# Kernel tuning notes

Hardware: AMD Instinct MI355X
Metric: run time of the kernel (lower is better)

Reference implementation:

```python
import math
import jax, jax.numpy as jnp
import numpy as np

B, N, D, H = 4, 2048, 512, 8
HD = D // H


def setup_inputs() -> dict:
    key = jax.random.key(0)
    ks = jax.random.split(key, 7)
    w_scale = 1.0 / math.sqrt(D)  # keep logits in a sane range (like default init)
    return {
        "q": jax.random.normal(ks[0], (B, N, D), dtype=jnp.float32),
        "mask": jax.random.randint(ks[1], (B, N), 0, 2) == 1,  # True = masked key
        "attn_bias": jax.random.normal(ks[2], (B, N, N), dtype=jnp.float32),
        "Wq": jax.random.normal(ks[3], (D, D), dtype=jnp.float32) * w_scale,
        "Wk": jax.random.normal(ks[4], (D, D), dtype=jnp.float32) * w_scale,
        "Wv": jax.random.normal(ks[5], (D, D), dtype=jnp.float32) * w_scale,
        "Wo": jax.random.normal(ks[6], (D, D), dtype=jnp.float32) * w_scale,
    }


def _heads(v):
    # [B, N, D] -> [H, B, N, HD]  (mirrors reshape + movedim(-2, 0))
    b, n, d = v.shape
    return v.reshape(b, n, H, HD).transpose(2, 0, 1, 3)


def reference(q, mask, attn_bias, Wq, Wk, Wv, Wo):
    # Linear projections (torch Linear: x @ W.T)
    qh = _heads(q @ Wq.T)
    kh = _heads(q @ Wk.T)   # self-attention: h defaults to q
    vh = _heads(q @ Wv.T)
    # scores: [H, B, Nq, Nk]
    scores = jnp.einsum("hbqd,hbkd->hbqk", qh, kh) / math.sqrt(HD)
    scores = scores + attn_bias[None]                     # broadcast over heads
    scores = jnp.where(mask[None, :, None, :], -jnp.inf, scores)
    attn = jax.nn.softmax(scores, axis=-1)
    out = jnp.einsum("hbqk,hbkd->hbqd", attn, vh)         # [H, B, Nq, HD]
    out = out.transpose(1, 2, 0, 3).reshape(q.shape[0], q.shape[1], D)
    return out @ Wo.T
```

## Files before the change

kernel.cpp:

```cpp
#include <hip/hip_runtime.h>
#include <stdint.h>


typedef __attribute__((ext_vector_type(8))) short short8;
typedef __attribute__((ext_vector_type(4))) short short4v;
typedef __attribute__((ext_vector_type(4))) float f32x4;

#define DEV static __device__ __forceinline__

constexpr int Bc = 4, Nc = 2048, Dc = 512, Hc = 8, HDc = 64;
constexpr int Mc = Bc * Nc;
constexpr int QKVNc = 3 * Dc;
constexpr float L2E = 1.44269504f;

DEV short bf16cast(float f) {
  return (short)__builtin_bit_cast(unsigned short, (__bf16)f);
}
DEV unsigned cvt_pk_bf16(float a, float b) {
  unsigned short lb = __builtin_bit_cast(unsigned short, (__bf16)a);
  unsigned short hb = __builtin_bit_cast(unsigned short, (__bf16)b);
  return (unsigned)lb | ((unsigned)hb << 16);
}
DEV unsigned pack_shorts(short a, short b) {
  return (unsigned)(unsigned short)a | ((unsigned)(unsigned short)b << 16);
}
DEV short8 cvt8(float4 a, float4 b) {
  union { short8 s; uint4 u; } r;
  r.u.x = cvt_pk_bf16(a.x, a.y); r.u.y = cvt_pk_bf16(a.z, a.w);
  r.u.z = cvt_pk_bf16(b.x, b.y); r.u.w = cvt_pk_bf16(b.z, b.w);
  return r.s;
}
DEV float fast_exp2(float x) {
#if __has_builtin(__builtin_amdgcn_exp2f)
  return __builtin_amdgcn_exp2f(x);
#else
  return exp2f(x);
#endif
}
DEV void permswap32(unsigned& a, unsigned& b) {
  asm volatile("v_permlane32_swap_b32 %0, %1" : "+v"(a), "+v"(b));
}

__global__ void cvtw_kernel(const float* __restrict__ Wq, const float* __restrict__ Wk,
                            const float* __restrict__ Wv, const float* __restrict__ Wo,
                            short* __restrict__ Wqkv, short* __restrict__ Wob,
                            const void* __restrict__ mask, float* __restrict__ mf) {
  if (blockIdx.x == 1024) {
    __shared__ int flag;
    if (threadIdx.x == 0) flag = 0;
    __syncthreads();
    const uchar4* m4 = (const uchar4*)mask;
    int acc = 0;
    for (int i = threadIdx.x; i < 2048; i += 256) {
      uchar4 v = m4[i];
      acc |= (int)v.y | (int)v.z | (int)v.w;
    }
    if (acc) atomicOr(&flag, 1);
    __syncthreads();
    int isbyte = flag;
    for (int i = threadIdx.x; i < Bc * Nc; i += 256) {
      int v = isbyte ? (int)((const unsigned char*)mask)[i] : ((const int*)mask)[i];
      mf[i] = v ? -1e30f : 0.0f;
    }
    return;
  }
  int which = blockIdx.x >> 8;
  int j = (blockIdx.x & 255) * 256 + threadIdx.x;
  const float* src = which == 0 ? Wq : which == 1 ? Wk : which == 2 ? Wv : Wo;
  short* dst = (which == 3) ? Wob : Wqkv + which * (Dc * Dc);
  float4 v = ((const float4*)src)[j];
  short4v o = { bf16cast(v.x), bf16cast(v.y), bf16cast(v.z), bf16cast(v.w) };
  ((short4v*)dst)[j] = o;
}

template<bool A_F32, bool OUT_F32>
__global__ __launch_bounds__(256, 2) void gemm_bt(const void* __restrict__ Av,
                                                  const short* __restrict__ Bm,
                                                  void* __restrict__ Cv,
                                                  int M, int N, int K,
                                                  int qcols, float cscale) {
  __shared__ __align__(16) short At[128 * 72];
  __shared__ __align__(16) short Bt[128 * 72];
  const int tid = threadIdx.x, lane = tid & 63, wv = tid >> 6;
  const int quad = lane >> 4, l16 = lane & 15;
  const int mbase = blockIdx.y * 128, nbase = blockIdx.x * 128;
  const int wr = (wv >> 1) * 64, wc = (wv & 1) * 64;
  const float scale = (nbase < qcols) ? cscale : 1.0f;
  f32x4 acc[4][4] = {};
  float4 apf[4][2]; short8 aph[4], bpre[4];
#pragma unroll
  for (int i = 0; i < 4; i++) {
    int flat = i * 256 + tid, row = flat >> 3, ch8 = (flat & 7) * 8;
    if (A_F32) {
      const float* Af = (const float*)Av;
      apf[i][0] = *(const float4*)&Af[(size_t)(mbase + row) * K + ch8];
      apf[i][1] = *(const float4*)&Af[(size_t)(mbase + row) * K + ch8 + 4];
    } else {
      aph[i] = *(const short8*)&((const short*)Av)[(size_t)(mbase + row) * K + ch8];
    }
    bpre[i] = *(const short8*)&Bm[(size_t)(nbase + row) * K + ch8];
  }
  for (int k0 = 0; k0 < K; k0 += 64) {
    __syncthreads();
#pragma unroll
    for (int i = 0; i < 4; i++) {
      int flat = i * 256 + tid, row = flat >> 3, ch8 = (flat & 7) * 8;
      *(short8*)&At[row * 72 + ch8] = A_F32 ? cvt8(apf[i][0], apf[i][1]) : aph[i];
      *(short8*)&Bt[row * 72 + ch8] = bpre[i];
    }
    if (k0 + 64 < K) {
#pragma unroll
      for (int i = 0; i < 4; i++) {
        int flat = i * 256 + tid, row = flat >> 3, ch8 = (flat & 7) * 8;
        if (A_F32) {
          const float* Af = (const float*)Av;
          apf[i][0] = *(const float4*)&Af[(size_t)(mbase + row) * K + k0 + 64 + ch8];
          apf[i][1] = *(const float4*)&Af[(size_t)(mbase + row) * K + k0 + 64 + ch8 + 4];
        } else {
          aph[i] = *(const short8*)&((const short*)Av)[(size_t)(mbase + row) * K + k0 + 64 + ch8];
        }
        bpre[i] = *(const short8*)&Bm[(size_t)(nbase + row) * K + k0 + 64 + ch8];
      }
    }
    __syncthreads();
#pragma unroll
    for (int s = 0; s < 2; s++) {
      short8 af[4], bf[4];
#pragma unroll
      for (int t = 0; t < 4; t++) {
        af[t] = *(short8*)&At[(wr + t * 16 + l16) * 72 + quad * 8 + s * 32];
        bf[t] = *(short8*)&Bt[(wc + t * 16 + l16) * 72 + quad * 8 + s * 32];
      }
#pragma unroll
      for (int mt = 0; mt < 4; mt++)
#pragma unroll
        for (int nt = 0; nt < 4; nt++)
          acc[mt][nt] = __builtin_amdgcn_mfma_f32_16x16x32_bf16(af[mt], bf[nt], acc[mt][nt], 0, 0, 0);
    }
  }
#pragma unroll
  for (int mt = 0; mt < 4; mt++)
#pragma unroll
    for (int nt = 0; nt < 4; nt++)
#pragma unroll
      for (int r = 0; r < 4; r++) {
        int row = mbase + wr + mt * 16 + quad * 4 + r;
        int col = nbase + wc + nt * 16 + l16;
        float v = acc[mt][nt][r] * scale;
        if (OUT_F32) ((float*)Cv)[(size_t)row * N + col] = v;
        else         ((short*)Cv)[(size_t)row * N + col] = bf16cast(v);
      }
}

__global__ __launch_bounds__(512, 2) void attn_kernel(const short* __restrict__ QKV,
                                                      const float* __restrict__ bias,
                                                      const float* __restrict__ maskf,
                                                      short* __restrict__ Aout) {
  __shared__ __align__(16) short Kt[2][64 * 64];
  __shared__ __align__(16) short Vt[2][64 * 64];
  __shared__ __align__(16) float mlds[Nc];
  const int tid = threadIdx.x, lane = tid & 63, wv = tid >> 6;
  const int quad = lane >> 4, l16 = lane & 15;
  const int qt = blockIdx.x & 15, h = (blockIdx.x >> 4) & 7, b = (int)(blockIdx.x >> 7);
  const int qrow0 = qt * 128;
  const int qglob = qrow0 + wv * 16 + l16;
  const float* biasrow = bias + ((size_t)b * Nc + qglob) * Nc;

  ((float4*)mlds)[tid] = ((const float4*)(maskf + b * Nc))[tid];

  short8 qf[2];
  {
    const short* qp = QKV + (size_t)(b * Nc + qglob) * QKVNc + h * HDc + quad * 8;
    qf[0] = *(const short8*)qp;
    qf[1] = *(const short8*)(qp + 32);
  }

  const int vp = tid & 31, vq = tid >> 5;
  const int vperm = (vp & 25) | ((vp & 4) >> 1) | ((vp & 2) << 1);
  const int krow = tid >> 3, kchunk = tid & 7;
  const int kwofs = krow * 64 + ((kchunk ^ (krow & 7)) << 3);
  const short* Kbase = QKV + Dc + h * HDc;
  const short* Vbase = QKV + 2 * Dc + h * HDc;

  short8 kpre; short4v v0pre, v1pre; float4 bpre[4];
  kpre  = *(const short8*)&Kbase[(size_t)(b * Nc + krow) * QKVNc + kchunk * 8];
  v0pre = *(const short4v*)&Vbase[(size_t)(b * Nc + 2 * vp) * QKVNc + 4 * vq];
  v1pre = *(const short4v*)&Vbase[(size_t)(b * Nc + 2 * vp + 1) * QKVNc + 4 * vq];
#pragma unroll
  for (int t = 0; t < 4; t++) bpre[t] = *(const float4*)&biasrow[t * 16 + quad * 4];

  const short ONEB = (short)0x3F80;
  const short8 ones = { ONEB, ONEB, ONEB, ONEB, ONEB, ONEB, ONEB, ONEB };

  f32x4 oacc[4] = {};
  f32x4 sumacc = {};

  for (int kt = 0; kt < 32; kt++) {
    const int cur = kt & 1;
    const int kb = kt * 64;
    const int kbn = ((kt + 1) & 31) * 64;

    *(short8*)&Kt[cur][kwofs] = kpre;
#pragma unroll
    for (int j = 0; j < 4; j++) {
      int hd = 4 * vq + j;
      *(unsigned*)&Vt[cur][hd * 64 + (((vperm >> 2) ^ (hd & 7)) << 3) + 2 * (vperm & 3)] =
          pack_shorts(v0pre[j], v1pre[j]);
    }
    __syncthreads();

    f32x4 sacc[4];
#pragma unroll
    for (int t = 0; t < 4; t++) {
      float4 mv = *(const float4*)&mlds[kb + t * 16 + quad * 4];
      sacc[t][0] = __builtin_fmaf(bpre[t].x, L2E, mv.x);
      sacc[t][1] = __builtin_fmaf(bpre[t].y, L2E, mv.y);
      sacc[t][2] = __builtin_fmaf(bpre[t].z, L2E, mv.z);
      sacc[t][3] = __builtin_fmaf(bpre[t].w, L2E, mv.w);
    }

    kpre  = *(const short8*)&Kbase[(size_t)(b * Nc + kbn + krow) * QKVNc + kchunk * 8];
    v0pre = *(const short4v*)&Vbase[(size_t)(b * Nc + kbn + 2 * vp) * QKVNc + 4 * vq];
    v1pre = *(const short4v*)&Vbase[(size_t)(b * Nc + kbn + 2 * vp + 1) * QKVNc + 4 * vq];
#pragma unroll
    for (int t = 0; t < 4; t++) bpre[t] = *(const float4*)&biasrow[kbn + t * 16 + quad * 4];

#pragma unroll
    for (int s = 0; s < 2; s++)
#pragma unroll
      for (int t = 0; t < 4; t++) {
        short8 kf = *(short8*)&Kt[cur][(t * 16 + l16) * 64 + (((quad + 4 * s) ^ (l16 & 7)) << 3)];
        sacc[t] = __builtin_amdgcn_mfma_f32_16x16x32_bf16(kf, qf[s], sacc[t], 0, 0, 0);
      }

    unsigned pw[4][2];
#pragma unroll
    for (int t = 0; t < 4; t++) {
      float p0 = fast_exp2(sacc[t][0]);
      float p1 = fast_exp2(sacc[t][1]);
      float p2 = fast_exp2(sacc[t][2]);
      float p3 = fast_exp2(sacc[t][3]);
      pw[t][0] = cvt_pk_bf16(p0, p1);
      pw[t][1] = cvt_pk_bf16(p2, p3);
    }
    permswap32(pw[0][0], pw[1][0]); permswap32(pw[0][1], pw[1][1]);
    permswap32(pw[2][0], pw[3][0]); permswap32(pw[2][1], pw[3][1]);
    union { unsigned u[4]; short8 s; }
        pf0{{pw[0][0], pw[0][1], pw[1][0], pw[1][1]}},
        pf1{{pw[2][0], pw[2][1], pw[3][0], pw[3][1]}};

#pragma unroll
    for (int s = 0; s < 2; s++) {
      short8 pf = s ? pf1.s : pf0.s;
      sumacc = __builtin_amdgcn_mfma_f32_16x16x32_bf16(pf, ones, sumacc, 0, 0, 0);
#pragma unroll
      for (int t = 0; t < 4; t++) {
        short8 vf = *(short8*)&Vt[cur][(t * 16 + l16) * 64 + (((quad + 4 * s) ^ (l16 & 7)) << 3)];
        oacc[t] = __builtin_amdgcn_mfma_f32_16x16x32_bf16(pf, vf, oacc[t], 0, 0, 0);
      }
    }
  }

#pragma unroll
  for (int r = 0; r < 4; r++) {
    float inv = 1.0f / sumacc[r];
    int row = b * Nc + qrow0 + wv * 16 + quad * 4 + r;
#pragma unroll
    for (int t = 0; t < 4; t++)
      Aout[(size_t)row * Dc + h * HDc + t * 16 + l16] = bf16cast(oacc[t][r] * inv);
  }
}

extern "C" void kernel_launch(void* const* d_in, const int* in_sizes, int n_in,
                              void* d_out, int out_size, void* d_ws, size_t ws_size,
                              hipStream_t stream) {
  const float* q    = (const float*)d_in[0];
  const void*  mask = d_in[1];
  const float* bias = (const float*)d_in[2];
  const float* Wq   = (const float*)d_in[3];
  const float* Wk   = (const float*)d_in[4];
  const float* Wv   = (const float*)d_in[5];
  const float* Wo   = (const float*)d_in[6];
  float* out = (float*)d_out;

  char* ws = (char*)d_ws;
  short* Wqkv = (short*)ws;  ws += (size_t)QKVNc * Dc * 2;
  short* Wob  = (short*)ws;  ws += (size_t)Dc * Dc * 2;
  float* mf   = (float*)ws;  ws += (size_t)Bc * Nc * 4;
  short* QKV  = (short*)ws;  ws += (size_t)Mc * QKVNc * 2;
  short* aout = (short*)ws;  ws += (size_t)Mc * Dc * 2;

  cvtw_kernel<<<dim3(1025), dim3(256), 0, stream>>>(Wq, Wk, Wv, Wo, Wqkv, Wob, mask, mf);

  gemm_bt<true, false><<<dim3(QKVNc / 128, Mc / 128), dim3(256), 0, stream>>>(
      (const void*)q, Wqkv, (void*)QKV, Mc, QKVNc, Dc, Dc, 0.125f * L2E);
  attn_kernel<<<dim3(Bc * Hc * 16), dim3(512), 0, stream>>>(QKV, bias, mf, aout);
  gemm_bt<false, true><<<dim3(Dc / 128, Mc / 128), dim3(256), 0, stream>>>(
      (const void*)aout, Wob, (void*)out, Mc, Dc, Dc, 0, 1.0f);
}
```

Baseline: 276.9 us.

## Process two query sub-tiles per wave in attention, halving block threads

The attention kernel now runs 4 waves of 256 threads, each handling 32 query rows as two 16-row MFMA sub-tiles, so each K/V fragment read from LDS feeds two MFMAs. K/V staging loads are widened to 16-byte vectors per thread. Bias loads are no longer prefetched one iteration ahead but issued inside the loop after the barrier, and the bias add moves after the QK MFMA. Mask preparation is split into its own single-block kernel. This raises register pressure and drops bias prefetch latency hiding, which can reduce occupancy or stall on the bias stream.

```diff
diff --git a/kernel.cpp b/kernel.cpp
--- a/kernel.cpp
+++ b/kernel.cpp
@@ -43,27 +43,7 @@
 
 __global__ void cvtw_kernel(const float* __restrict__ Wq, const float* __restrict__ Wk,
                             const float* __restrict__ Wv, const float* __restrict__ Wo,
-                            short* __restrict__ Wqkv, short* __restrict__ Wob,
-                            const void* __restrict__ mask, float* __restrict__ mf) {
-  if (blockIdx.x == 1024) {
-    __shared__ int flag;
-    if (threadIdx.x == 0) flag = 0;
-    __syncthreads();
-    const uchar4* m4 = (const uchar4*)mask;
-    int acc = 0;
-    for (int i = threadIdx.x; i < 2048; i += 256) {
-      uchar4 v = m4[i];
-      acc |= (int)v.y | (int)v.z | (int)v.w;
-    }
-    if (acc) atomicOr(&flag, 1);
-    __syncthreads();
-    int isbyte = flag;
-    for (int i = threadIdx.x; i < Bc * Nc; i += 256) {
-      int v = isbyte ? (int)((const unsigned char*)mask)[i] : ((const int*)mask)[i];
-      mf[i] = v ? -1e30f : 0.0f;
-    }
-    return;
-  }
+                            short* __restrict__ Wqkv, short* __restrict__ Wob) {
   int which = blockIdx.x >> 8;
   int j = (blockIdx.x & 255) * 256 + threadIdx.x;
   const float* src = which == 0 ? Wq : which == 1 ? Wk : which == 2 ? Wv : Wo;
@@ -71,6 +51,25 @@
   float4 v = ((const float4*)src)[j];
   short4v o = { bf16cast(v.x), bf16cast(v.y), bf16cast(v.z), bf16cast(v.w) };
   ((short4v*)dst)[j] = o;
+}
+
+__global__ void maskprep_kernel(const void* __restrict__ mask, float* __restrict__ mf) {
+  __shared__ int flag;
+  if (threadIdx.x == 0) flag = 0;
+  __syncthreads();
+  const uchar4* m4 = (const uchar4*)mask;
+  int acc = 0;
+  for (int i = threadIdx.x; i < 2048; i += 1024) {
+    uchar4 v = m4[i];
+    acc |= (int)v.y | (int)v.z | (int)v.w;
+  }
+  if (acc) atomicOr(&flag, 1);
+  __syncthreads();
+  int isbyte = flag;
+  for (int i = threadIdx.x; i < Bc * Nc; i += 1024) {
+    int v = isbyte ? (int)((const unsigned char*)mask)[i] : ((const int*)mask)[i];
+    mf[i] = v ? -1e30f : 0.0f;
+  }
 }
 
 template<bool A_F32, bool OUT_F32>
@@ -152,7 +151,7 @@
       }
 }
 
-__global__ __launch_bounds__(512, 2) void attn_kernel(const short* __restrict__ QKV,
+__global__ __launch_bounds__(256, 2) void attn_kernel(const short* __restrict__ QKV,
                                                       const float* __restrict__ bias,
                                                       const float* __restrict__ maskf,
                                                       short* __restrict__ Aout) {
@@ -163,112 +162,137 @@
   const int quad = lane >> 4, l16 = lane & 15;
   const int qt = blockIdx.x & 15, h = (blockIdx.x >> 4) & 7, b = (int)(blockIdx.x >> 7);
   const int qrow0 = qt * 128;
-  const int qglob = qrow0 + wv * 16 + l16;
-  const float* biasrow = bias + ((size_t)b * Nc + qglob) * Nc;
-
-  ((float4*)mlds)[tid] = ((const float4*)(maskf + b * Nc))[tid];
-
-  short8 qf[2];
+  const int q0 = qrow0 + wv * 32 + l16;
+  const float* biasq0 = bias + ((size_t)b * Nc + q0) * Nc;
+  const float* biasq1 = biasq0 + (size_t)16 * Nc;
+
+  ((float4*)mlds)[tid]       = ((const float4*)(maskf + b * Nc))[tid];
+  ((float4*)mlds)[tid + 256] = ((const float4*)(maskf + b * Nc))[tid + 256];
+
+  short8 qf[2][2];
   {
-    const short* qp = QKV + (size_t)(b * Nc + qglob) * QKVNc + h * HDc + quad * 8;
-    qf[0] = *(const short8*)qp;
-    qf[1] = *(const short8*)(qp + 32);
-  }
-
+    const short* qp0 = QKV + (size_t)(b * Nc + q0) * QKVNc + h * HDc + quad * 8;
+    qf[0][0] = *(const short8*)qp0;
+    qf[0][1] = *(const short8*)(qp0 + 32);
+    const short* qp1 = qp0 + (size_t)16 * QKVNc;
+    qf[1][0] = *(const short8*)qp1;
+    qf[1][1] = *(const short8*)(qp1 + 32);
+  }
+
+  const int krow = tid >> 2, kch0 = (tid & 3) * 2;
+  const int kw0 = krow * 64 + ((kch0 ^ (krow & 7)) << 3);
+  const int kw1 = krow * 64 + (((kch0 + 1) ^ (krow & 7)) << 3);
   const int vp = tid & 31, vq = tid >> 5;
   const int vperm = (vp & 25) | ((vp & 4) >> 1) | ((vp & 2) << 1);
-  const int krow = tid >> 3, kchunk = tid & 7;
-  const int kwofs = krow * 64 + ((kchunk ^ (krow & 7)) << 3);
+  const int vwbase = (((vperm >> 2)) << 3) + 2 * (vperm & 3);
   const short* Kbase = QKV + Dc + h * HDc;
   const short* Vbase = QKV + 2 * Dc + h * HDc;
 
-  short8 kpre; short4v v0pre, v1pre; float4 bpre[4];
-  kpre  = *(const short8*)&Kbase[(size_t)(b * Nc + krow) * QKVNc + kchunk * 8];
-  v0pre = *(const short4v*)&Vbase[(size_t)(b * Nc + 2 * vp) * QKVNc + 4 * vq];
-  v1pre = *(const short4v*)&Vbase[(size_t)(b * Nc + 2 * vp + 1) * QKVNc + 4 * vq];
-#pragma unroll
-  for (int t = 0; t < 4; t++) bpre[t] = *(const float4*)&biasrow[t * 16 + quad * 4];
+  short8 kpre0, kpre1, v0pre, v1pre;
+  {
+    const short* kp = &Kbase[(size_t)(b * Nc + krow) * QKVNc + kch0 * 8];
+    kpre0 = *(const short8*)kp;
+    kpre1 = *(const short8*)(kp + 8);
+    v0pre = *(const short8*)&Vbase[(size_t)(b * Nc + 2 * vp) * QKVNc + vq * 8];
+    v1pre = *(const short8*)&Vbase[(size_t)(b * Nc + 2 * vp + 1) * QKVNc + vq * 8];
+  }
 
   const short ONEB = (short)0x3F80;
   const short8 ones = { ONEB, ONEB, ONEB, ONEB, ONEB, ONEB, ONEB, ONEB };
 
-  f32x4 oacc[4] = {};
-  f32x4 sumacc = {};
+  f32x4 oacc[2][4] = {};
+  f32x4 sumacc[2] = {};
 
   for (int kt = 0; kt < 32; kt++) {
     const int cur = kt & 1;
     const int kb = kt * 64;
     const int kbn = ((kt + 1) & 31) * 64;
 
-    *(short8*)&Kt[cur][kwofs] = kpre;
-#pragma unroll
-    for (int j = 0; j < 4; j++) {
-      int hd = 4 * vq + j;
-      *(unsigned*)&Vt[cur][hd * 64 + (((vperm >> 2) ^ (hd & 7)) << 3) + 2 * (vperm & 3)] =
+    *(short8*)&Kt[cur][kw0] = kpre0;
+    *(short8*)&Kt[cur][kw1] = kpre1;
+#pragma unroll
+    for (int j = 0; j < 8; j++) {
+      int hd = vq * 8 + j;
+      *(unsigned*)&Vt[cur][hd * 64 + (vwbase ^ ((hd & 7) << 3))] =
           pack_shorts(v0pre[j], v1pre[j]);
     }
     __syncthreads();
 
-    f32x4 sacc[4];
+    {
+      const short* kp = &Kbase[(size_t)(b * Nc + kbn + krow) * QKVNc + kch0 * 8];
+      kpre0 = *(const short8*)kp;
+      kpre1 = *(const short8*)(kp + 8);
+      v0pre = *(const short8*)&Vbase[(size_t)(b * Nc + kbn + 2 * vp) * QKVNc + vq * 8];
+      v1pre = *(const short8*)&Vbase[(size_t)(b * Nc + kbn + 2 * vp + 1) * QKVNc + vq * 8];
+    }
+    float4 bb[2][4];
+#pragma unroll
+    for (int t = 0; t < 4; t++) {
+      bb[0][t] = *(const float4*)&biasq0[kb + t * 16 + quad * 4];
+      bb[1][t] = *(const float4*)&biasq1[kb + t * 16 + quad * 4];
+    }
+
+    f32x4 sacc[2][4];
 #pragma unroll
     for (int t = 0; t < 4; t++) {
       float4 mv = *(const float4*)&mlds[kb + t * 16 + quad * 4];
-      sacc[t][0] = __builtin_fmaf(bpre[t].x, L2E, mv.x);
-      sacc[t][1] = __builtin_fmaf(bpre[t].y, L2E, mv.y);
-      sacc[t][2] = __builtin_fmaf(bpre[t].z, L2E, mv.z);
-      sacc[t][3] = __builtin_fmaf(bpre[t].w, L2E, mv.w);
-    }
-
-    kpre  = *(const short8*)&Kbase[(size_t)(b * Nc + kbn + krow) * QKVNc + kchunk * 8];
-    v0pre = *(const short4v*)&Vbase[(size_t)(b * Nc + kbn + 2 * vp) * QKVNc + 4 * vq];
-    v1pre = *(const short4v*)&Vbase[(size_t)(b * Nc + kbn + 2 * vp + 1) * QKVNc + 4 * vq];
-#pragma unroll
-    for (int t = 0; t < 4; t++) bpre[t] = *(const float4*)&biasrow[kbn + t * 16 + quad * 4];
+      sacc[0][t][0] = mv.x; sacc[0][t][1] = mv.y; sacc[0][t][2] = mv.z; sacc[0][t][3] = mv.w;
+      sacc[1][t] = sacc[0][t];
+    }
 
 #pragma unroll
     for (int s = 0; s < 2; s++)
 #pragma unroll
       for (int t = 0; t < 4; t++) {
         short8 kf = *(short8*)&Kt[cur][(t * 16 + l16) * 64 + (((quad + 4 * s) ^ (l16 & 7)) << 3)];
-        sacc[t] = __builtin_amdgcn_mfma_f32_16x16x32_bf16(kf, qf[s], sacc[t], 0, 0, 0);
-      }
-
-    unsigned pw[4][2];
-#pragma unroll
-    for (int t = 0; t < 4; t++) {
-      float p0 = fast_exp2(sacc[t][0]);
-      float p1 = fast_exp2(sacc[t][1]);
-      float p2 = fast_exp2(sacc[t][2]);
-      float p3 = fast_exp2(sacc[t][3]);
-      pw[t][0] = cvt_pk_bf16(p0, p1);
-      pw[t][1] = cvt_pk_bf16(p2, p3);
-    }
-    permswap32(pw[0][0], pw[1][0]); permswap32(pw[0][1], pw[1][1]);
-    permswap32(pw[2][0], pw[3][0]); permswap32(pw[2][1], pw[3][1]);
-    union { unsigned u[4]; short8 s; }
-        pf0{{pw[0][0], pw[0][1], pw[1][0], pw[1][1]}},
-        pf1{{pw[2][0], pw[2][1], pw[3][0], pw[3][1]}};
+        sacc[0][t] = __builtin_amdgcn_mfma_f32_16x16x32_bf16(kf, qf[0][s], sacc[0][t], 0, 0, 0);
+        sacc[1][t] = __builtin_amdgcn_mfma_f32_16x16x32_bf16(kf, qf[1][s], sacc[1][t], 0, 0, 0);
+      }
+
+    short8 pf[2][2];
+#pragma unroll
+    for (int n = 0; n < 2; n++) {
+      unsigned pw[4][2];
+#pragma unroll
+      for (int t = 0; t < 4; t++) {
+        float p0 = fast_exp2(__builtin_fmaf(bb[n][t].x, L2E, sacc[n][t][0]));
+        float p1 = fast_exp2(__builtin_fmaf(bb[n][t].y, L2E, sacc[n][t][1]));
+        float p2 = fast_exp2(__builtin_fmaf(bb[n][t].z, L2E, sacc[n][t][2]));
+        float p3 = fast_exp2(__builtin_fmaf(bb[n][t].w, L2E, sacc[n][t][3]));
+        pw[t][0] = cvt_pk_bf16(p0, p1);
+        pw[t][1] = cvt_pk_bf16(p2, p3);
+      }
+      permswap32(pw[0][0], pw[1][0]); permswap32(pw[0][1], pw[1][1]);
+      permswap32(pw[2][0], pw[3][0]); permswap32(pw[2][1], pw[3][1]);
+      union { unsigned u[4]; short8 s; }
+          a0{{pw[0][0], pw[0][1], pw[1][0], pw[1][1]}},
+          a1{{pw[2][0], pw[2][1], pw[3][0], pw[3][1]}};
+      pf[n][0] = a0.s; pf[n][1] = a1.s;
+    }
 
 #pragma unroll
     for (int s = 0; s < 2; s++) {
-      short8 pf = s ? pf1.s : pf0.s;
-      sumacc = __builtin_amdgcn_mfma_f32_16x16x32_bf16(pf, ones, sumacc, 0, 0, 0);
+      sumacc[0] = __builtin_amdgcn_mfma_f32_16x16x32_bf16(pf[0][s], ones, sumacc[0], 0, 0, 0);
+      sumacc[1] = __builtin_amdgcn_mfma_f32_16x16x32_bf16(pf[1][s], ones, sumacc[1], 0, 0, 0);
 #pragma unroll
       for (int t = 0; t < 4; t++) {
         short8 vf = *(short8*)&Vt[cur][(t * 16 + l16) * 64 + (((quad + 4 * s) ^ (l16 & 7)) << 3)];
-        oacc[t] = __builtin_amdgcn_mfma_f32_16x16x32_bf16(pf, vf, oacc[t], 0, 0, 0);
-      }
-    }
-  }
-
-#pragma unroll
-  for (int r = 0; r < 4; r++) {
-    float inv = 1.0f / sumacc[r];
-    int row = b * Nc + qrow0 + wv * 16 + quad * 4 + r;
-#pragma unroll
-    for (int t = 0; t < 4; t++)
-      Aout[(size_t)row * Dc + h * HDc + t * 16 + l16] = bf16cast(oacc[t][r] * inv);
-  }
+        oacc[0][t] = __builtin_amdgcn_mfma_f32_16x16x32_bf16(pf[0][s], vf, oacc[0][t], 0, 0, 0);
+        oacc[1][t] = __builtin_amdgcn_mfma_f32_16x16x32_bf16(pf[1][s], vf, oacc[1][t], 0, 0, 0);
+      }
+    }
+  }
+
+#pragma unroll
+  for (int m = 0; m < 2; m++)
+#pragma unroll
+    for (int r = 0; r < 4; r++) {
+      float inv = 1.0f / sumacc[m][r];
+      int row = b * Nc + qrow0 + wv * 32 + m * 16 + quad * 4 + r;
+#pragma unroll
+      for (int t = 0; t < 4; t++)
+        Aout[(size_t)row * Dc + h * HDc + t * 16 + l16] = bf16cast(oacc[m][t][r] * inv);
+    }
 }
 
 extern "C" void kernel_launch(void* const* d_in, const int* in_sizes, int n_in,
@@ -290,11 +314,12 @@
   short* QKV  = (short*)ws;  ws += (size_t)Mc * QKVNc * 2;
   short* aout = (short*)ws;  ws += (size_t)Mc * Dc * 2;
 
-  cvtw_kernel<<<dim3(1025), dim3(256), 0, stream>>>(Wq, Wk, Wv, Wo, Wqkv, Wob, mask, mf);
+  cvtw_kernel<<<dim3(1024), dim3(256), 0, stream>>>(Wq, Wk, Wv, Wo, Wqkv, Wob);
+  maskprep_kernel<<<dim3(1), dim3(1024), 0, stream>>>(mask, mf);
 
   gemm_bt<true, false><<<dim3(QKVNc / 128, Mc / 128), dim3(256), 0, stream>>>(
       (const void*)q, Wqkv, (void*)QKV, Mc, QKVNc, Dc, Dc, 0.125f * L2E);
-  attn_kernel<<<dim3(Bc * Hc * 16), dim3(512), 0, stream>>>(QKV, bias, mf, aout);
+  attn_kernel<<<dim3(Bc * Hc * 16), dim3(256), 0, stream>>>(QKV, bias, mf, aout);
   gemm_bt<false, true><<<dim3(Dc / 128, Mc / 128), dim3(256), 0, stream>>>(
       (const void*)aout, Wob, (void*)out, Mc, Dc, Dc, 0, 1.0f);
 }
```

Result: no change. 273.0 us (-1.4%).
